# Optimization experiments

Hardware: AMD Instinct MI355X
Metric: run time of the kernel (lower is better)

The kernel has to match this reference:

```python
import jax, jax.numpy as jnp
import numpy as np

H = 1024
E = 8
TOP_K = 2
B, S = 4, 2048


def setup_inputs() -> dict:
    key = jax.random.key(0)
    ks = jax.random.split(key, 8)
    scale = 0.02
    return {
        "x": jax.random.normal(ks[0], (B, S, H), dtype=jnp.float32),
        "router_w": jax.random.normal(ks[1], (H, E), dtype=jnp.float32) * scale,
        "router_b": jnp.zeros((E,), dtype=jnp.float32),
        "w1": jax.random.normal(ks[2], (E, H, 4 * H), dtype=jnp.float32) * scale,
        "b1": jnp.zeros((E, 4 * H), dtype=jnp.float32),
        "w2": jax.random.normal(ks[3], (E, 4 * H, H), dtype=jnp.float32) * scale,
        "b2": jnp.zeros((E, H), dtype=jnp.float32),
    }


def reference(x, router_w, router_b, w1, b1, w2, b2):
    b, s, h = x.shape
    n_exp = w1.shape[0]
    x_flat = x.reshape(-1, h)  # [T, H]
    T = x_flat.shape[0]

    # Router: softmax then top-k, renormalize top-k probs (matches torch code).
    logits = x_flat @ router_w + router_b            # [T, E]
    probs = jax.nn.softmax(logits, axis=-1)
    top_values, top_indices = jax.lax.top_k(probs, TOP_K)  # [T, k]
    top_values = top_values / jnp.sum(top_values, axis=-1, keepdims=True)

    # Per-token combine weight for each expert (0 if token not routed there).
    combine = jnp.zeros((T, n_exp), dtype=x.dtype)
    combine = combine.at[jnp.arange(T)[:, None], top_indices].add(top_values)  # [T, E]

    # Loop over the small fixed expert set; masked combine weights zero out
    # contributions from unrouted tokens, matching the gather/scatter original.
    out = jnp.zeros_like(x_flat)
    for e in range(n_exp):
        hmid = jax.nn.gelu(x_flat @ w1[e] + b1[e], approximate=False)  # [T, 4H]
        y = hmid @ w2[e] + b2[e]                                       # [T, H]
        out = out + combine[:, e:e + 1] * y
    return out.reshape(b, s, h)
```

## Files before the change

kernel.cpp:

```cpp
#include <hip/hip_runtime.h>
#include <hip/hip_bf16.h>
#include <math.h>

#define TT 8192
#define HD 1024
#define FHD 4096
#define NE 8
#define TMAX 72

typedef short s16x8 __attribute__((ext_vector_type(8)));
typedef float f32x4 __attribute__((ext_vector_type(4)));
using bf16 = __hip_bfloat16;
typedef unsigned int u32;

#define OFF_COUNTS 0
#define OFF_CURSOR 64
#define OFF_OFFS   128
#define OFF_E0     256
#define OFF_E1     (OFF_E0 + 4*TT)
#define OFF_W0     (OFF_E1 + 4*TT)
#define OFF_W1     (OFF_W0 + 4*TT)
#define OFF_S0     (OFF_W1 + 4*TT)
#define OFF_S1     (OFF_S0 + 4*TT)
#define OFF_TID    (OFF_S1 + 4*TT)
#define OFF_TW     (OFF_TID + 8*TT)
#define OFF_TMR    (OFF_TW + 8*TT)
#define OFF_TME    (OFF_TMR + 4*144)
#define OFF_TMN    (OFF_TME + 4*144)
#define OFF_XBF    (OFF_TMN + 64)
#define OFF_W1T    (OFF_XBF + 2*TT*HD)
#define OFF_W2T    (OFF_W1T + 2*NE*HD*FHD)
#define OFF_HMID   (OFF_W2T + 2*NE*HD*FHD)
#define OFF_YS     (OFF_HMID + (size_t)2*(2*TT)*FHD)

__device__ __forceinline__ void gload_lds16(const void* g, void* l) {
    __builtin_amdgcn_global_load_lds(
        (const __attribute__((address_space(1))) u32*)g,
        (__attribute__((address_space(3))) u32*)l, 16, 0, 0);
}

__global__ __launch_bounds__(256) void cast_x_kernel(const float* __restrict__ x, bf16* __restrict__ xbf) {
    int i = (blockIdx.x * 256 + threadIdx.x) * 8;
    float4 a = *reinterpret_cast<const float4*>(&x[i]);
    float4 b = *reinterpret_cast<const float4*>(&x[i + 4]);
    bf16 h[8];
    h[0] = __float2bfloat16(a.x); h[1] = __float2bfloat16(a.y);
    h[2] = __float2bfloat16(a.z); h[3] = __float2bfloat16(a.w);
    h[4] = __float2bfloat16(b.x); h[5] = __float2bfloat16(b.y);
    h[6] = __float2bfloat16(b.z); h[7] = __float2bfloat16(b.w);
    *reinterpret_cast<uint4*>(&xbf[i]) = *reinterpret_cast<uint4*>(h);
}

__global__ __launch_bounds__(256) void transpose_cast_kernel(const float* __restrict__ in,
        bf16* __restrict__ out, int R, int C) {
    __shared__ float tile[64][65];
    int rt = R >> 6, ct = C >> 6;
    int e = blockIdx.x / (rt * ct);
    int rem = blockIdx.x % (rt * ct);
    int r0 = (rem / ct) << 6, c0 = (rem % ct) << 6;
    const float* ine = in + (size_t)e * R * C;
    bf16* oute = out + (size_t)e * R * C;
    int tid = threadIdx.x;
#pragma unroll
    for (int i = 0; i < 4; ++i) {
        int lin = tid + i * 256;
        int r = lin >> 4, cg = lin & 15;
        float4 v = *reinterpret_cast<const float4*>(&ine[(size_t)(r0 + r) * C + c0 + cg * 4]);
        tile[r][cg * 4 + 0] = v.x; tile[r][cg * 4 + 1] = v.y;
        tile[r][cg * 4 + 2] = v.z; tile[r][cg * 4 + 3] = v.w;
    }
    __syncthreads();
#pragma unroll
    for (int i = 0; i < 4; ++i) {
        int lin = tid + i * 256;
        int n = lin >> 4, kg = lin & 15;
        bf16 h[4];
        h[0] = __float2bfloat16(tile[kg * 4 + 0][n]);
        h[1] = __float2bfloat16(tile[kg * 4 + 1][n]);
        h[2] = __float2bfloat16(tile[kg * 4 + 2][n]);
        h[3] = __float2bfloat16(tile[kg * 4 + 3][n]);
        *reinterpret_cast<uint2*>(&oute[(size_t)(c0 + n) * R + r0 + kg * 4]) =
            *reinterpret_cast<uint2*>(h);
    }
}

__global__ __launch_bounds__(256) void router_kernel(const float* __restrict__ x,
        const float* __restrict__ rw, const float* __restrict__ rb,
        int* __restrict__ e0a, int* __restrict__ e1a,
        float* __restrict__ w0a, float* __restrict__ w1a, int* __restrict__ counts) {
    int wid = threadIdx.x >> 6, lane = threadIdx.x & 63;
    int t = blockIdx.x * 4 + wid;
    const float* xp = x + (size_t)t * HD + lane * 16;
    float xv[16];
#pragma unroll
    for (int j = 0; j < 4; ++j) {
        float4 v = *reinterpret_cast<const float4*>(&xp[j * 4]);
        xv[4 * j] = v.x; xv[4 * j + 1] = v.y; xv[4 * j + 2] = v.z; xv[4 * j + 3] = v.w;
    }
    float acc[8] = {0.f, 0.f, 0.f, 0.f, 0.f, 0.f, 0.f, 0.f};
    const float* rp = rw + (size_t)(lane * 16) * NE;
#pragma unroll
    for (int hh = 0; hh < 16; ++hh) {
        float4 r0 = *reinterpret_cast<const float4*>(&rp[hh * 8]);
        float4 r1 = *reinterpret_cast<const float4*>(&rp[hh * 8 + 4]);
        acc[0] += xv[hh] * r0.x; acc[1] += xv[hh] * r0.y;
        acc[2] += xv[hh] * r0.z; acc[3] += xv[hh] * r0.w;
        acc[4] += xv[hh] * r1.x; acc[5] += xv[hh] * r1.y;
        acc[6] += xv[hh] * r1.z; acc[7] += xv[hh] * r1.w;
    }
#pragma unroll
    for (int e = 0; e < 8; ++e) {
#pragma unroll
        for (int off = 32; off > 0; off >>= 1) acc[e] += __shfl_xor(acc[e], off, 64);
    }
    if (lane == 0) {
        float lg[8];
#pragma unroll
        for (int e = 0; e < 8; ++e) lg[e] = acc[e] + rb[e];
        int a = 0;
#pragma unroll
        for (int e = 1; e < 8; ++e) if (lg[e] > lg[a]) a = e;
        int b = (a == 0) ? 1 : 0;
#pragma unroll
        for (int e = 0; e < 8; ++e) if (e != a && e != b && lg[e] > lg[b]) b = e;
        float wa = 1.0f / (1.0f + expf(lg[b] - lg[a]));
        float wb = 1.0f / (1.0f + expf(lg[a] - lg[b]));
        e0a[t] = a; e1a[t] = b; w0a[t] = wa; w1a[t] = wb;
        atomicAdd(&counts[a], 1);
        atomicAdd(&counts[b], 1);
    }
}

__global__ void scan_offsets_kernel(const int* __restrict__ counts, int* __restrict__ offs,
        int* __restrict__ cursor, int* __restrict__ tmr, int* __restrict__ tme,
        int* __restrict__ tmn) {
    if (threadIdx.x == 0 && blockIdx.x == 0) {
        int s = 0, nt = 0;
        for (int e = 0; e < NE; ++e) {
            offs[e] = s; cursor[e] = s;
            int c = counts[e];
            for (int j = 0; j < c; j += 256) { tmr[nt] = s + j; tme[nt] = e; ++nt; }
            s += c;
        }
        offs[NE] = s;
        tmn[0] = nt;
        for (int i = nt; i < TMAX; ++i) { tmr[i] = 0; tme[i] = 0; }
    }
}

__global__ __launch_bounds__(256) void scatter_kernel(const int* __restrict__ e0a, const int* __restrict__ e1a,
        const float* __restrict__ w0a, const float* __restrict__ w1a,
        int* __restrict__ cursor, int* __restrict__ tid_arr, float* __restrict__ tw_arr,
        int* __restrict__ slot0, int* __restrict__ slot1) {
    int t = blockIdx.x * 256 + threadIdx.x;
    int s0 = atomicAdd(&cursor[e0a[t]], 1);
    tid_arr[s0] = t; tw_arr[s0] = w0a[t]; slot0[t] = s0;
    int s1 = atomicAdd(&cursor[e1a[t]], 1);
    tid_arr[s1] = t; tw_arr[s1] = w1a[t]; slot1[t] = s1;
}

__global__ __launch_bounds__(512) void gemm1_kernel(const bf16* __restrict__ xbf, const bf16* __restrict__ w1t,
        const float* __restrict__ b1, const int* __restrict__ offs,
        const int* __restrict__ tid_arr, bf16* __restrict__ hmid,
        const int* __restrict__ tmr, const int* __restrict__ tme, const int* __restrict__ tmn) {
    __shared__ bf16 As[4 * 256 * 32];
    __shared__ bf16 Bs[4 * 256 * 32];
    __shared__ int toks[256];
    int nwg = gridDim.x;
    int orig = blockIdx.x;
    int wg = (orig & 7) * (nwg >> 3) + (orig >> 3);
    int nt = wg / TMAX, tidx = wg % TMAX;
    if (tidx >= tmn[0]) return;
    int e = tme[tidx], row0 = tmr[tidx], s1 = offs[e + 1];
    int n0 = nt * 256;
    int t = threadIdx.x;
    if (t < 256) { int s = row0 + t; toks[t] = tid_arr[(s < s1) ? s : (s1 - 1)]; }
    __syncthreads();
    int lane = t & 63, w = t >> 6;
    const bf16* w1e = w1t + (size_t)e * FHD * HD;
    int rs = t >> 2, g = t & 3;
    int swz = (g ^ ((rs >> 1) & 3)) * 8;
    const bf16* srcA0 = xbf + (size_t)toks[rs] * HD + swz;
    const bf16* srcA1 = xbf + (size_t)toks[rs + 128] * HD + swz;
    const bf16* srcB0 = w1e + (size_t)(n0 + rs) * HD + swz;
    const bf16* srcB1 = w1e + (size_t)(n0 + rs + 128) * HD + swz;
    int dst0 = w * 512;
    int dst1 = 4096 + w * 512;
    int wr = w >> 2, wc = w & 3;
    int lr = lane & 15, lk = (lane >> 4) * 8;
    int offA[8], offB[4];
#pragma unroll
    for (int m = 0; m < 8; ++m) { int row = wr * 128 + m * 16 + lr; offA[m] = row * 32 + (lk ^ (8 * ((row >> 1) & 3))); }
#pragma unroll
    for (int n = 0; n < 4; ++n) { int row = wc * 64 + n * 16 + lr; offB[n] = row * 32 + (lk ^ (8 * ((row >> 1) & 3))); }
    f32x4 acc[8][4] = {};
#pragma unroll
    for (int kt = 0; kt < 3; ++kt) {
        int bo = kt * 8192, ko = kt * 32;
        gload_lds16(srcA0 + ko, &As[bo + dst0]);
        gload_lds16(srcA1 + ko, &As[bo + dst1]);
        gload_lds16(srcB0 + ko, &Bs[bo + dst0]);
        gload_lds16(srcB1 + ko, &Bs[bo + dst1]);
    }
    asm volatile("s_waitcnt vmcnt(8)" ::: "memory");
    __builtin_amdgcn_s_barrier();
    for (int kt = 0; kt < HD / 32; ++kt) {
        const bf16* Ab = &As[(kt & 3) * 8192];
        const bf16* Bb = &Bs[(kt & 3) * 8192];
        s16x8 aF[8], bF[4];
#pragma unroll
        for (int m = 0; m < 8; ++m) aF[m] = *reinterpret_cast<const s16x8*>(&Ab[offA[m]]);
#pragma unroll
        for (int n = 0; n < 4; ++n) bF[n] = *reinterpret_cast<const s16x8*>(&Bb[offB[n]]);
        int kt3 = kt + 3; if (kt3 >= HD / 32) kt3 -= HD / 32;
        int bo = (kt3 & 3) * 8192, ko = kt3 * 32;
        gload_lds16(srcA0 + ko, &As[bo + dst0]);
        gload_lds16(srcA1 + ko, &As[bo + dst1]);
        gload_lds16(srcB0 + ko, &Bs[bo + dst0]);
        gload_lds16(srcB1 + ko, &Bs[bo + dst1]);
        asm volatile("s_waitcnt vmcnt(8)" ::: "memory");
        __builtin_amdgcn_s_barrier();
        __builtin_amdgcn_sched_barrier(0);
        __builtin_amdgcn_s_setprio(1);
#pragma unroll
        for (int m = 0; m < 8; ++m)
#pragma unroll
            for (int n = 0; n < 4; ++n)
                acc[m][n] = __builtin_amdgcn_mfma_f32_16x16x32_bf16(aF[m], bF[n], acc[m][n], 0, 0, 0);
        __builtin_amdgcn_s_setprio(0);
        __builtin_amdgcn_sched_barrier(0);
        __builtin_amdgcn_s_barrier();
    }
#pragma unroll
    for (int n = 0; n < 4; ++n) {
        int col = n0 + wc * 64 + n * 16 + lr;
        float bv = b1[(size_t)e * FHD + col];
#pragma unroll
        for (int m = 0; m < 8; ++m) {
#pragma unroll
            for (int r = 0; r < 4; ++r) {
                int row = wr * 128 + m * 16 + (lane >> 4) * 4 + r;
                int slot = row0 + row;
                if (slot < s1) {
                    float v2 = acc[m][n][r] + bv;
                    v2 = 0.5f * v2 * (1.0f + erff(v2 * 0.70710678118f));
                    hmid[(size_t)slot * FHD + col] = __float2bfloat16(v2);
                }
            }
        }
    }
}

__global__ __launch_bounds__(512) void gemm2_kernel(const bf16* __restrict__ hmid, const bf16* __restrict__ w2t,
        const float* __restrict__ b2, const int* __restrict__ offs, float* __restrict__ ys,
        const int* __restrict__ tmr, const int* __restrict__ tme, const int* __restrict__ tmn) {
    __shared__ bf16 As[4 * 256 * 32];
    __shared__ bf16 Bs[4 * 128 * 32];
    int nwg = gridDim.x;
    int orig = blockIdx.x;
    int wg = (orig & 7) * (nwg >> 3) + (orig >> 3);
    int nt = wg / TMAX, tidx = wg % TMAX;
    if (tidx >= tmn[0]) return;
    int e = tme[tidx], row0 = tmr[tidx], s1 = offs[e + 1];
    int n0 = nt * 128;
    int t = threadIdx.x;
    int lane = t & 63, w = t >> 6;
    const bf16* w2e = w2t + (size_t)e * HD * FHD;
    int rs = t >> 2, g = t & 3;
    int swz = (g ^ ((rs >> 1) & 3)) * 8;
    int ar0 = row0 + rs;       if (ar0 >= s1) ar0 = s1 - 1;
    int ar1 = row0 + rs + 128; if (ar1 >= s1) ar1 = s1 - 1;
    const bf16* srcA0 = hmid + (size_t)ar0 * FHD + swz;
    const bf16* srcA1 = hmid + (size_t)ar1 * FHD + swz;
    const bf16* srcB0 = w2e + (size_t)(n0 + rs) * FHD + swz;
    int dstA0 = w * 512;
    int dstA1 = 4096 + w * 512;
    int dstB  = w * 512;
    int wr = w >> 1, wc = w & 1;
    int lr = lane & 15, lk = (lane >> 4) * 8;
    int offA[4], offB[4];
#pragma unroll
    for (int m = 0; m < 4; ++m) { int row = wr * 64 + m * 16 + lr; offA[m] = row * 32 + (lk ^ (8 * ((row >> 1) & 3))); }
#pragma unroll
    for (int n = 0; n < 4; ++n) { int row = wc * 64 + n * 16 + lr; offB[n] = row * 32 + (lk ^ (8 * ((row >> 1) & 3))); }
    f32x4 acc[4][4] = {};
#pragma unroll
    for (int kt = 0; kt < 3; ++kt) {
        int boA = kt * 8192, boB = kt * 4096, ko = kt * 32;
        gload_lds16(srcA0 + ko, &As[boA + dstA0]);
        gload_lds16(srcA1 + ko, &As[boA + dstA1]);
        gload_lds16(srcB0 + ko, &Bs[boB + dstB]);
    }
    asm volatile("s_waitcnt vmcnt(6)" ::: "memory");
    __builtin_amdgcn_s_barrier();
    for (int kt = 0; kt < FHD / 32; ++kt) {
        const bf16* Ab = &As[(kt & 3) * 8192];
        const bf16* Bb = &Bs[(kt & 3) * 4096];
        s16x8 aF[4], bF[4];
#pragma unroll
        for (int m = 0; m < 4; ++m) aF[m] = *reinterpret_cast<const s16x8*>(&Ab[offA[m]]);
#pragma unroll
        for (int n = 0; n < 4; ++n) bF[n] = *reinterpret_cast<const s16x8*>(&Bb[offB[n]]);
        int kt3 = kt + 3; if (kt3 >= FHD / 32) kt3 -= FHD / 32;
        int boA = (kt3 & 3) * 8192, boB = (kt3 & 3) * 4096, ko = kt3 * 32;
        gload_lds16(srcA0 + ko, &As[boA + dstA0]);
        gload_lds16(srcA1 + ko, &As[boA + dstA1]);
        gload_lds16(srcB0 + ko, &Bs[boB + dstB]);
        asm volatile("s_waitcnt vmcnt(6)" ::: "memory");
        __builtin_amdgcn_s_barrier();
        __builtin_amdgcn_sched_barrier(0);
        __builtin_amdgcn_s_setprio(1);
#pragma unroll
        for (int m = 0; m < 4; ++m)
#pragma unroll
            for (int n = 0; n < 4; ++n)
                acc[m][n] = __builtin_amdgcn_mfma_f32_16x16x32_bf16(aF[m], bF[n], acc[m][n], 0, 0, 0);
        __builtin_amdgcn_s_setprio(0);
        __builtin_amdgcn_sched_barrier(0);
        __builtin_amdgcn_s_barrier();
    }
#pragma unroll
    for (int n = 0; n < 4; ++n) {
        int col = n0 + wc * 64 + n * 16 + lr;
        float bv = b2[(size_t)e * HD + col];
#pragma unroll
        for (int m = 0; m < 4; ++m) {
#pragma unroll
            for (int r = 0; r < 4; ++r) {
                int row = wr * 64 + m * 16 + (lane >> 4) * 4 + r;
                int slot = row0 + row;
                if (slot < s1) ys[(size_t)slot * HD + col] = acc[m][n][r] + bv;
            }
        }
    }
}

__global__ __launch_bounds__(256) void combine_kernel(const float* __restrict__ ys,
        const int* __restrict__ slot0, const int* __restrict__ slot1,
        const float* __restrict__ tw, float* __restrict__ out) {
    int t = blockIdx.x;
    int c = threadIdx.x * 4;
    int sa = slot0[t], sb = slot1[t];
    float wa = tw[sa], wb = tw[sb];
    float4 a = *reinterpret_cast<const float4*>(&ys[(size_t)sa * HD + c]);
    float4 b = *reinterpret_cast<const float4*>(&ys[(size_t)sb * HD + c]);
    float4 o;
    o.x = wa * a.x + wb * b.x; o.y = wa * a.y + wb * b.y;
    o.z = wa * a.z + wb * b.z; o.w = wa * a.w + wb * b.w;
    *reinterpret_cast<float4*>(&out[(size_t)t * HD + c]) = o;
}

extern "C" void kernel_launch(void* const* d_in, const int* in_sizes, int n_in,
                              void* d_out, int out_size, void* d_ws, size_t ws_size,
                              hipStream_t stream) {
    const float* x  = (const float*)d_in[0];
    const float* rw = (const float*)d_in[1];
    const float* rb = (const float*)d_in[2];
    const float* w1 = (const float*)d_in[3];
    const float* b1 = (const float*)d_in[4];
    const float* w2 = (const float*)d_in[5];
    const float* b2 = (const float*)d_in[6];
    float* out = (float*)d_out;
    char* ws = (char*)d_ws;

    int*   counts  = (int*)(ws + OFF_COUNTS);
    int*   cursor  = (int*)(ws + OFF_CURSOR);
    int*   offs    = (int*)(ws + OFF_OFFS);
    int*   e0a     = (int*)(ws + OFF_E0);
    int*   e1a     = (int*)(ws + OFF_E1);
    float* w0a     = (float*)(ws + OFF_W0);
    float* w1a     = (float*)(ws + OFF_W1);
    int*   slot0   = (int*)(ws + OFF_S0);
    int*   slot1   = (int*)(ws + OFF_S1);
    int*   tid_arr = (int*)(ws + OFF_TID);
    float* tw_arr  = (float*)(ws + OFF_TW);
    int*   tmr     = (int*)(ws + OFF_TMR);
    int*   tme     = (int*)(ws + OFF_TME);
    int*   tmn     = (int*)(ws + OFF_TMN);
    bf16*  xbf     = (bf16*)(ws + OFF_XBF);
    bf16*  w1t     = (bf16*)(ws + OFF_W1T);
    bf16*  w2t     = (bf16*)(ws + OFF_W2T);
    bf16*  hmid    = (bf16*)(ws + OFF_HMID);
    float* ys      = (float*)(ws + OFF_YS);

    hipMemsetAsync(counts, 0, 64, stream);

    cast_x_kernel<<<TT * HD / 2048, 256, 0, stream>>>(x, xbf);
    transpose_cast_kernel<<<NE * (HD / 64) * (FHD / 64), 256, 0, stream>>>(w1, w1t, HD, FHD);
    transpose_cast_kernel<<<NE * (FHD / 64) * (HD / 64), 256, 0, stream>>>(w2, w2t, FHD, HD);
    router_kernel<<<TT / 4, 256, 0, stream>>>(x, rw, rb, e0a, e1a, w0a, w1a, counts);
    scan_offsets_kernel<<<1, 64, 0, stream>>>(counts, offs, cursor, tmr, tme, tmn);
    scatter_kernel<<<TT / 256, 256, 0, stream>>>(e0a, e1a, w0a, w1a, cursor, tid_arr, tw_arr, slot0, slot1);
    gemm1_kernel<<<(FHD / 256) * TMAX, 512, 0, stream>>>(xbf, w1t, b1, offs, tid_arr, hmid, tmr, tme, tmn);
    gemm2_kernel<<<(HD / 128) * TMAX, 512, 0, stream>>>(hmid, w2t, b2, offs, ys, tmr, tme, tmn);
    combine_kernel<<<TT, 256, 0, stream>>>(ys, slot0, slot1, tw_arr, out);
}
```

Baseline: 968.9 us.

## Restructure expert GEMMs into 8-wave quadrant ping-pong pipeline with split-K gemm2

Both grouped GEMMs are rewritten to use a 256x256 tile with BK=64, double-buffered LDS split into halves, and four interleaved phases per k-step in which LDS reads, global-to-LDS staging and MFMA quadrants overlap. gemm2 moves from 256x128 tiles to 256x256 tiles with a 2-way split over K, writing two partial outputs that the combine kernel sums. The second partial buffer reuses the w1t workspace region, which is dead after gemm1. The goals are more MFMA work per barrier and better memory latency hiding, at the cost of extra partial-output traffic and higher register pressure from __launch_bounds__(512,2).

```diff
diff --git a/kernel.cpp b/kernel.cpp
--- a/kernel.cpp
+++ b/kernel.cpp
@@ -159,12 +159,45 @@
     tid_arr[s1] = t; tw_arr[s1] = w1a[t]; slot1[t] = s1;
 }
 
-__global__ __launch_bounds__(512) void gemm1_kernel(const bf16* __restrict__ xbf, const bf16* __restrict__ w1t,
-        const float* __restrict__ b1, const int* __restrict__ offs,
-        const int* __restrict__ tid_arr, bf16* __restrict__ hmid,
-        const int* __restrict__ tmr, const int* __restrict__ tme, const int* __restrict__ tmn) {
-    __shared__ bf16 As[4 * 256 * 32];
-    __shared__ bf16 Bs[4 * 256 * 32];
+#define STG_A(H, KT) do { int _d = (KT) & 1; int _ko = (KT) * 64; \
+    gload_lds16(pA[H][0] + _ko, &As[_d][H][sd0]); \
+    gload_lds16(pA[H][1] + _ko, &As[_d][H][sd1]); } while (0)
+#define STG_B(H, KT) do { int _d = (KT) & 1; int _ko = (KT) * 64; \
+    gload_lds16(pB[H][0] + _ko, &Bs[_d][H][sd0]); \
+    gload_lds16(pB[H][1] + _ko, &Bs[_d][H][sd1]); } while (0)
+#define RD_A(H, D) do { _Pragma("unroll") for (int mi = 0; mi < 4; ++mi) { \
+    af[mi][0] = *reinterpret_cast<const s16x8*>(&As[D][H][(rab + mi * 16) * 64 + koff0]); \
+    af[mi][1] = *reinterpret_cast<const s16x8*>(&As[D][H][(rab + mi * 16) * 64 + koff1]); } } while (0)
+#define RD_B(H, D) do { _Pragma("unroll") for (int ni = 0; ni < 2; ++ni) { \
+    bfr[ni][0] = *reinterpret_cast<const s16x8*>(&Bs[D][H][(cbb + ni * 16) * 64 + koff0]); \
+    bfr[ni][1] = *reinterpret_cast<const s16x8*>(&Bs[D][H][(cbb + ni * 16) * 64 + koff1]); } } while (0)
+#define MFMA_Q(MH, NH) do { _Pragma("unroll") for (int mi = 0; mi < 4; ++mi) \
+    _Pragma("unroll") for (int ni = 0; ni < 2; ++ni) \
+    _Pragma("unroll") for (int ks = 0; ks < 2; ++ks) \
+      acc[(MH)*4+mi][(NH)*2+ni] = __builtin_amdgcn_mfma_f32_16x16x32_bf16( \
+          af[mi][ks], bfr[ni][ks], acc[(MH)*4+mi][(NH)*2+ni], 0, 0, 0); } while (0)
+#define PH_MID() \
+    __builtin_amdgcn_s_barrier(); \
+    asm volatile("s_waitcnt lgkmcnt(0)" ::: "memory"); \
+    __builtin_amdgcn_sched_barrier(0); \
+    __builtin_amdgcn_s_setprio(1);
+#define PH_END_W() \
+    __builtin_amdgcn_s_setprio(0); \
+    __builtin_amdgcn_sched_barrier(0); \
+    asm volatile("s_waitcnt vmcnt(4)" ::: "memory"); \
+    __builtin_amdgcn_s_barrier();
+#define PH_END_NW() \
+    __builtin_amdgcn_s_setprio(0); \
+    __builtin_amdgcn_sched_barrier(0); \
+    __builtin_amdgcn_s_barrier();
+
+__global__ __launch_bounds__(512, 2) void gemm1_kernel(const bf16* __restrict__ xbf,
+        const bf16* __restrict__ w1t, const float* __restrict__ b1,
+        const int* __restrict__ offs, const int* __restrict__ tid_arr,
+        bf16* __restrict__ hmid, const int* __restrict__ tmr,
+        const int* __restrict__ tme, const int* __restrict__ tmn) {
+    __shared__ bf16 As[2][2][8192];
+    __shared__ bf16 Bs[2][2][8192];
     __shared__ int toks[256];
     int nwg = gridDim.x;
     int orig = blockIdx.x;
@@ -177,72 +210,61 @@
     if (t < 256) { int s = row0 + t; toks[t] = tid_arr[(s < s1) ? s : (s1 - 1)]; }
     __syncthreads();
     int lane = t & 63, w = t >> 6;
+    int wr = w >> 2, wc = w & 3;
+    int lr = lane & 15, kg = lane >> 4;
+    int rab = 64 * wr + lr;
+    int cbb = 32 * wc + lr;
+    int koff0 = (kg * 8) ^ ((lr & 7) << 3);
+    int koff1 = (32 + kg * 8) ^ ((lr & 7) << 3);
+    int l3 = lane >> 3, oct = lane & 7;
+    int rstage = w * 8 + l3;
+    int socts = (oct ^ l3) * 8;
     const bf16* w1e = w1t + (size_t)e * FHD * HD;
-    int rs = t >> 2, g = t & 3;
-    int swz = (g ^ ((rs >> 1) & 3)) * 8;
-    const bf16* srcA0 = xbf + (size_t)toks[rs] * HD + swz;
-    const bf16* srcA1 = xbf + (size_t)toks[rs + 128] * HD + swz;
-    const bf16* srcB0 = w1e + (size_t)(n0 + rs) * HD + swz;
-    const bf16* srcB1 = w1e + (size_t)(n0 + rs + 128) * HD + swz;
-    int dst0 = w * 512;
-    int dst1 = 4096 + w * 512;
-    int wr = w >> 2, wc = w & 3;
-    int lr = lane & 15, lk = (lane >> 4) * 8;
-    int offA[8], offB[4];
-#pragma unroll
-    for (int m = 0; m < 8; ++m) { int row = wr * 128 + m * 16 + lr; offA[m] = row * 32 + (lk ^ (8 * ((row >> 1) & 3))); }
-#pragma unroll
-    for (int n = 0; n < 4; ++n) { int row = wc * 64 + n * 16 + lr; offB[n] = row * 32 + (lk ^ (8 * ((row >> 1) & 3))); }
+    const bf16* pA[2][2]; const bf16* pB[2][2];
+#pragma unroll
+    for (int h = 0; h < 2; ++h)
+#pragma unroll
+        for (int j = 0; j < 2; ++j) {
+            int gr = j * 128 + h * 64 + rstage;
+            pA[h][j] = xbf + (size_t)toks[gr] * HD + socts;
+            int cb = rstage + j * 64;
+            int col = ((cb >> 5) << 6) + h * 32 + (cb & 31);
+            pB[h][j] = w1e + (size_t)(n0 + col) * HD + socts;
+        }
+    int sd0 = rstage * 64 + oct * 8;
+    int sd1 = sd0 + 4096;
     f32x4 acc[8][4] = {};
-#pragma unroll
-    for (int kt = 0; kt < 3; ++kt) {
-        int bo = kt * 8192, ko = kt * 32;
-        gload_lds16(srcA0 + ko, &As[bo + dst0]);
-        gload_lds16(srcA1 + ko, &As[bo + dst1]);
-        gload_lds16(srcB0 + ko, &Bs[bo + dst0]);
-        gload_lds16(srcB1 + ko, &Bs[bo + dst1]);
-    }
-    asm volatile("s_waitcnt vmcnt(8)" ::: "memory");
+    s16x8 af[4][2], bfr[2][2];
+    STG_A(0, 0); STG_B(0, 0); STG_B(1, 0); STG_A(1, 0);
+    asm volatile("s_waitcnt vmcnt(4)" ::: "memory");
     __builtin_amdgcn_s_barrier();
-    for (int kt = 0; kt < HD / 32; ++kt) {
-        const bf16* Ab = &As[(kt & 3) * 8192];
-        const bf16* Bb = &Bs[(kt & 3) * 8192];
-        s16x8 aF[8], bF[4];
-#pragma unroll
-        for (int m = 0; m < 8; ++m) aF[m] = *reinterpret_cast<const s16x8*>(&Ab[offA[m]]);
-#pragma unroll
-        for (int n = 0; n < 4; ++n) bF[n] = *reinterpret_cast<const s16x8*>(&Bb[offB[n]]);
-        int kt3 = kt + 3; if (kt3 >= HD / 32) kt3 -= HD / 32;
-        int bo = (kt3 & 3) * 8192, ko = kt3 * 32;
-        gload_lds16(srcA0 + ko, &As[bo + dst0]);
-        gload_lds16(srcA1 + ko, &As[bo + dst1]);
-        gload_lds16(srcB0 + ko, &Bs[bo + dst0]);
-        gload_lds16(srcB1 + ko, &Bs[bo + dst1]);
-        asm volatile("s_waitcnt vmcnt(8)" ::: "memory");
-        __builtin_amdgcn_s_barrier();
-        __builtin_amdgcn_sched_barrier(0);
-        __builtin_amdgcn_s_setprio(1);
-#pragma unroll
-        for (int m = 0; m < 8; ++m)
-#pragma unroll
-            for (int n = 0; n < 4; ++n)
-                acc[m][n] = __builtin_amdgcn_mfma_f32_16x16x32_bf16(aF[m], bF[n], acc[m][n], 0, 0, 0);
-        __builtin_amdgcn_s_setprio(0);
-        __builtin_amdgcn_sched_barrier(0);
-        __builtin_amdgcn_s_barrier();
-    }
-#pragma unroll
-    for (int n = 0; n < 4; ++n) {
-        int col = n0 + wc * 64 + n * 16 + lr;
-        float bv = b1[(size_t)e * FHD + col];
-#pragma unroll
-        for (int m = 0; m < 8; ++m) {
+    for (int kt = 0; kt < HD / 64; ++kt) {
+        int d = kt & 1, kn = kt + 1;
+        RD_A(0, d); RD_B(0, d);
+        STG_A(0, kn);
+        PH_MID(); MFMA_Q(0, 0); PH_END_W();
+        RD_B(1, d);
+        STG_B(0, kn);
+        PH_MID(); MFMA_Q(0, 1); PH_END_W();
+        RD_A(1, d);
+        STG_B(1, kn);
+        PH_MID(); MFMA_Q(1, 1); PH_END_NW();
+        RD_B(0, d);
+        STG_A(1, kn);
+        PH_MID(); MFMA_Q(1, 0); PH_END_W();
+    }
+#pragma unroll
+    for (int m8 = 0; m8 < 8; ++m8) {
+#pragma unroll
+        for (int ni = 0; ni < 4; ++ni) {
+            int col = n0 + wc * 64 + ni * 16 + lr;
+            float bv = b1[(size_t)e * FHD + col];
 #pragma unroll
             for (int r = 0; r < 4; ++r) {
-                int row = wr * 128 + m * 16 + (lane >> 4) * 4 + r;
+                int row = wr * 128 + m8 * 16 + kg * 4 + r;
                 int slot = row0 + row;
                 if (slot < s1) {
-                    float v2 = acc[m][n][r] + bv;
+                    float v2 = acc[m8][ni][r] + bv;
                     v2 = 0.5f * v2 * (1.0f + erff(v2 * 0.70710678118f));
                     hmid[(size_t)slot * FHD + col] = __float2bfloat16(v2);
                 }
@@ -251,102 +273,101 @@
     }
 }
 
-__global__ __launch_bounds__(512) void gemm2_kernel(const bf16* __restrict__ hmid, const bf16* __restrict__ w2t,
-        const float* __restrict__ b2, const int* __restrict__ offs, float* __restrict__ ys,
+__global__ __launch_bounds__(512, 2) void gemm2_kernel(const bf16* __restrict__ hmid,
+        const bf16* __restrict__ w2t, const float* __restrict__ b2,
+        const int* __restrict__ offs, float* __restrict__ ysA, float* __restrict__ ysB,
         const int* __restrict__ tmr, const int* __restrict__ tme, const int* __restrict__ tmn) {
-    __shared__ bf16 As[4 * 256 * 32];
-    __shared__ bf16 Bs[4 * 128 * 32];
+    __shared__ bf16 As[2][2][8192];
+    __shared__ bf16 Bs[2][2][8192];
     int nwg = gridDim.x;
     int orig = blockIdx.x;
     int wg = (orig & 7) * (nwg >> 3) + (orig >> 3);
-    int nt = wg / TMAX, tidx = wg % TMAX;
+    int gq = wg / TMAX, tidx = wg % TMAX;
     if (tidx >= tmn[0]) return;
+    int ks = gq >> 2, nt = gq & 3;
     int e = tme[tidx], row0 = tmr[tidx], s1 = offs[e + 1];
-    int n0 = nt * 128;
+    int n0 = nt * 256;
+    int kb = ks * 2048;
     int t = threadIdx.x;
     int lane = t & 63, w = t >> 6;
+    int wr = w >> 2, wc = w & 3;
+    int lr = lane & 15, kg = lane >> 4;
+    int rab = 64 * wr + lr;
+    int cbb = 32 * wc + lr;
+    int koff0 = (kg * 8) ^ ((lr & 7) << 3);
+    int koff1 = (32 + kg * 8) ^ ((lr & 7) << 3);
+    int l3 = lane >> 3, oct = lane & 7;
+    int rstage = w * 8 + l3;
+    int socts = (oct ^ l3) * 8;
     const bf16* w2e = w2t + (size_t)e * HD * FHD;
-    int rs = t >> 2, g = t & 3;
-    int swz = (g ^ ((rs >> 1) & 3)) * 8;
-    int ar0 = row0 + rs;       if (ar0 >= s1) ar0 = s1 - 1;
-    int ar1 = row0 + rs + 128; if (ar1 >= s1) ar1 = s1 - 1;
-    const bf16* srcA0 = hmid + (size_t)ar0 * FHD + swz;
-    const bf16* srcA1 = hmid + (size_t)ar1 * FHD + swz;
-    const bf16* srcB0 = w2e + (size_t)(n0 + rs) * FHD + swz;
-    int dstA0 = w * 512;
-    int dstA1 = 4096 + w * 512;
-    int dstB  = w * 512;
-    int wr = w >> 1, wc = w & 1;
-    int lr = lane & 15, lk = (lane >> 4) * 8;
-    int offA[4], offB[4];
-#pragma unroll
-    for (int m = 0; m < 4; ++m) { int row = wr * 64 + m * 16 + lr; offA[m] = row * 32 + (lk ^ (8 * ((row >> 1) & 3))); }
-#pragma unroll
-    for (int n = 0; n < 4; ++n) { int row = wc * 64 + n * 16 + lr; offB[n] = row * 32 + (lk ^ (8 * ((row >> 1) & 3))); }
-    f32x4 acc[4][4] = {};
-#pragma unroll
-    for (int kt = 0; kt < 3; ++kt) {
-        int boA = kt * 8192, boB = kt * 4096, ko = kt * 32;
-        gload_lds16(srcA0 + ko, &As[boA + dstA0]);
-        gload_lds16(srcA1 + ko, &As[boA + dstA1]);
-        gload_lds16(srcB0 + ko, &Bs[boB + dstB]);
-    }
-    asm volatile("s_waitcnt vmcnt(6)" ::: "memory");
+    const bf16* pA[2][2]; const bf16* pB[2][2];
+#pragma unroll
+    for (int h = 0; h < 2; ++h)
+#pragma unroll
+        for (int j = 0; j < 2; ++j) {
+            int ar = row0 + j * 128 + h * 64 + rstage;
+            if (ar >= s1) ar = s1 - 1;
+            pA[h][j] = hmid + (size_t)ar * FHD + kb + socts;
+            int cb = rstage + j * 64;
+            int col = ((cb >> 5) << 6) + h * 32 + (cb & 31);
+            pB[h][j] = w2e + (size_t)(n0 + col) * FHD + kb + socts;
+        }
+    int sd0 = rstage * 64 + oct * 8;
+    int sd1 = sd0 + 4096;
+    f32x4 acc[8][4] = {};
+    s16x8 af[4][2], bfr[2][2];
+    STG_A(0, 0); STG_B(0, 0); STG_B(1, 0); STG_A(1, 0);
+    asm volatile("s_waitcnt vmcnt(4)" ::: "memory");
     __builtin_amdgcn_s_barrier();
-    for (int kt = 0; kt < FHD / 32; ++kt) {
-        const bf16* Ab = &As[(kt & 3) * 8192];
-        const bf16* Bb = &Bs[(kt & 3) * 4096];
-        s16x8 aF[4], bF[4];
-#pragma unroll
-        for (int m = 0; m < 4; ++m) aF[m] = *reinterpret_cast<const s16x8*>(&Ab[offA[m]]);
-#pragma unroll
-        for (int n = 0; n < 4; ++n) bF[n] = *reinterpret_cast<const s16x8*>(&Bb[offB[n]]);
-        int kt3 = kt + 3; if (kt3 >= FHD / 32) kt3 -= FHD / 32;
-        int boA = (kt3 & 3) * 8192, boB = (kt3 & 3) * 4096, ko = kt3 * 32;
-        gload_lds16(srcA0 + ko, &As[boA + dstA0]);
-        gload_lds16(srcA1 + ko, &As[boA + dstA1]);
-        gload_lds16(srcB0 + ko, &Bs[boB + dstB]);
-        asm volatile("s_waitcnt vmcnt(6)" ::: "memory");
-        __builtin_amdgcn_s_barrier();
-        __builtin_amdgcn_sched_barrier(0);
-        __builtin_amdgcn_s_setprio(1);
-#pragma unroll
-        for (int m = 0; m < 4; ++m)
-#pragma unroll
-            for (int n = 0; n < 4; ++n)
-                acc[m][n] = __builtin_amdgcn_mfma_f32_16x16x32_bf16(aF[m], bF[n], acc[m][n], 0, 0, 0);
-        __builtin_amdgcn_s_setprio(0);
-        __builtin_amdgcn_sched_barrier(0);
-        __builtin_amdgcn_s_barrier();
-    }
-#pragma unroll
-    for (int n = 0; n < 4; ++n) {
-        int col = n0 + wc * 64 + n * 16 + lr;
-        float bv = b2[(size_t)e * HD + col];
-#pragma unroll
-        for (int m = 0; m < 4; ++m) {
+    for (int kt = 0; kt < 2048 / 64; ++kt) {
+        int d = kt & 1, kn = kt + 1;
+        RD_A(0, d); RD_B(0, d);
+        STG_A(0, kn);
+        PH_MID(); MFMA_Q(0, 0); PH_END_W();
+        RD_B(1, d);
+        STG_B(0, kn);
+        PH_MID(); MFMA_Q(0, 1); PH_END_W();
+        RD_A(1, d);
+        STG_B(1, kn);
+        PH_MID(); MFMA_Q(1, 1); PH_END_NW();
+        RD_B(0, d);
+        STG_A(1, kn);
+        PH_MID(); MFMA_Q(1, 0); PH_END_W();
+    }
+    float* ysp = ks ? ysB : ysA;
+#pragma unroll
+    for (int m8 = 0; m8 < 8; ++m8) {
+#pragma unroll
+        for (int ni = 0; ni < 4; ++ni) {
+            int col = n0 + wc * 64 + ni * 16 + lr;
+            float bv = ks ? 0.0f : b2[(size_t)e * HD + col];
 #pragma unroll
             for (int r = 0; r < 4; ++r) {
-                int row = wr * 64 + m * 16 + (lane >> 4) * 4 + r;
+                int row = wr * 128 + m8 * 16 + kg * 4 + r;
                 int slot = row0 + row;
-                if (slot < s1) ys[(size_t)slot * HD + col] = acc[m][n][r] + bv;
+                if (slot < s1) ysp[(size_t)slot * HD + col] = acc[m8][ni][r] + bv;
             }
         }
     }
 }
 
-__global__ __launch_bounds__(256) void combine_kernel(const float* __restrict__ ys,
+__global__ __launch_bounds__(256) void combine_kernel(const float* __restrict__ ysA,
+        const float* __restrict__ ysB,
         const int* __restrict__ slot0, const int* __restrict__ slot1,
         const float* __restrict__ tw, float* __restrict__ out) {
     int t = blockIdx.x;
     int c = threadIdx.x * 4;
     int sa = slot0[t], sb = slot1[t];
     float wa = tw[sa], wb = tw[sb];
-    float4 a = *reinterpret_cast<const float4*>(&ys[(size_t)sa * HD + c]);
-    float4 b = *reinterpret_cast<const float4*>(&ys[(size_t)sb * HD + c]);
+    float4 a0 = *reinterpret_cast<const float4*>(&ysA[(size_t)sa * HD + c]);
+    float4 a1 = *reinterpret_cast<const float4*>(&ysB[(size_t)sa * HD + c]);
+    float4 b0 = *reinterpret_cast<const float4*>(&ysA[(size_t)sb * HD + c]);
+    float4 b1 = *reinterpret_cast<const float4*>(&ysB[(size_t)sb * HD + c]);
     float4 o;
-    o.x = wa * a.x + wb * b.x; o.y = wa * a.y + wb * b.y;
-    o.z = wa * a.z + wb * b.z; o.w = wa * a.w + wb * b.w;
+    o.x = wa * (a0.x + a1.x) + wb * (b0.x + b1.x);
+    o.y = wa * (a0.y + a1.y) + wb * (b0.y + b1.y);
+    o.z = wa * (a0.z + a1.z) + wb * (b0.z + b1.z);
+    o.w = wa * (a0.w + a1.w) + wb * (b0.w + b1.w);
     *reinterpret_cast<float4*>(&out[(size_t)t * HD + c]) = o;
 }
 
@@ -381,7 +402,8 @@
     bf16*  w1t     = (bf16*)(ws + OFF_W1T);
     bf16*  w2t     = (bf16*)(ws + OFF_W2T);
     bf16*  hmid    = (bf16*)(ws + OFF_HMID);
-    float* ys      = (float*)(ws + OFF_YS);
+    float* ysA     = (float*)(ws + OFF_YS);
+    float* ysB     = (float*)(ws + OFF_W1T);
 
     hipMemsetAsync(counts, 0, 64, stream);
 
@@ -392,6 +414,6 @@
     scan_offsets_kernel<<<1, 64, 0, stream>>>(counts, offs, cursor, tmr, tme, tmn);
     scatter_kernel<<<TT / 256, 256, 0, stream>>>(e0a, e1a, w0a, w1a, cursor, tid_arr, tw_arr, slot0, slot1);
     gemm1_kernel<<<(FHD / 256) * TMAX, 512, 0, stream>>>(xbf, w1t, b1, offs, tid_arr, hmid, tmr, tme, tmn);
-    gemm2_kernel<<<(HD / 128) * TMAX, 512, 0, stream>>>(hmid, w2t, b2, offs, ys, tmr, tme, tmn);
-    combine_kernel<<<TT, 256, 0, stream>>>(ys, slot0, slot1, tw_arr, out);
-}
+    gemm2_kernel<<<2 * (HD / 256) * TMAX, 512, 0, stream>>>(hmid, w2t, b2, offs, ysA, ysB, tmr, tme, tmn);
+    combine_kernel<<<TT, 256, 0, stream>>>(ysA, ysB, slot0, slot1, tw_arr, out);
+}
```

Result: no change. 980.4 us (+1.2%).
